# Kernel tuning notes

Hardware: AMD Instinct MI355X
Metric: run time of the kernel (lower is better)

The kernel has to match this reference:

```python
import jax, jax.numpy as jnp
import numpy as np

EPS = 1e-5


def ternarize(w):
    # TWN: delta = 0.7*mean|w|; alpha = mean of |w| over entries above delta
    delta = 0.7 * jnp.mean(jnp.abs(w))
    mask = (jnp.abs(w) > delta).astype(w.dtype)
    alpha = jnp.sum(jnp.abs(w) * mask) / jnp.maximum(jnp.sum(mask), 1.0)
    q = alpha * jnp.sign(w) * mask
    # straight-through estimator (matches torch `w + (q - w).detach()`)
    return w + jax.lax.stop_gradient(q - w)


def conv2d(x, w, stride, pad):
    # x: NCHW, w: OIHW
    return jax.lax.conv_general_dilated(
        x, w, window_strides=(stride, stride), padding=[(pad, pad), (pad, pad)],
        dimension_numbers=("NCHW", "OIHW", "NCHW"))


def batchnorm(x, gamma, beta, mean, var):
    # inference-mode BN over channel dim of NCHW
    inv = gamma / jnp.sqrt(var + EPS)
    return x * inv[None, :, None, None] + (beta - mean * inv)[None, :, None, None]


def setup_inputs() -> dict:
    key = jax.random.key(0)
    ks = jax.random.split(key, 12)
    d = {
        "x": jax.random.normal(ks[0], (64, 3, 224, 224), jnp.float32),
        "w1": jax.random.normal(ks[1], (32, 3, 3, 3), jnp.float32) * 0.1,
        "g1": jnp.ones((32,), jnp.float32), "b1": jnp.zeros((32,), jnp.float32),
        "m1": jax.random.normal(ks[2], (32,), jnp.float32) * 0.1,
        "v1": jax.random.uniform(ks[3], (32,), jnp.float32, 0.5, 1.5),
        "w2": jax.random.normal(ks[4], (64, 32, 3, 3), jnp.float32) * 0.05,
        "g2": jnp.ones((64,), jnp.float32), "b2": jnp.zeros((64,), jnp.float32),
        "m2": jax.random.normal(ks[5], (64,), jnp.float32) * 0.1,
        "v2": jax.random.uniform(ks[6], (64,), jnp.float32, 0.5, 1.5),
        "w3": jax.random.normal(ks[7], (128, 64, 3, 3), jnp.float32) * 0.05,
        "g3": jnp.ones((128,), jnp.float32), "b3": jnp.zeros((128,), jnp.float32),
        "m3": jax.random.normal(ks[8], (128,), jnp.float32) * 0.1,
        "v3": jax.random.uniform(ks[9], (128,), jnp.float32, 0.5, 1.5),
        "wl": jax.random.normal(ks[10], (10, 128), jnp.float32) * 0.1,
        "bl": jax.random.normal(ks[11], (10,), jnp.float32) * 0.01,
    }
    return d


def reference(x, w1, g1, b1, m1, v1, w2, g2, b2, m2, v2,
              w3, g3, b3, m3, v3, wl, bl):
    h = jax.nn.relu(batchnorm(conv2d(x, ternarize(w1), 2, 1), g1, b1, m1, v1))
    h = jax.nn.relu(batchnorm(conv2d(h, ternarize(w2), 1, 1), g2, b2, m2, v2))
    h = jax.nn.relu(batchnorm(conv2d(h, ternarize(w3), 2, 1), g3, b3, m3, v3))
    h = jnp.mean(h, axis=(2, 3))  # AdaptiveAvgPool2d((1,1)) + flatten -> [N,128]
    return h @ ternarize(wl).T + bl
```

## Files before the change

kernel.cpp:

```cpp
#include <hip/hip_runtime.h>
#include <cstddef>

typedef __attribute__((ext_vector_type(8))) short short8;
typedef __attribute__((ext_vector_type(4))) float floatx4;

__device__ __forceinline__ unsigned short f2bf(float f) {
  union { float f; unsigned u; } v; v.f = f;
  const unsigned r = v.u + 0x7fffu + ((v.u >> 16) & 1u);
  return (unsigned short)(r >> 16);
}

__device__ __forceinline__ float block_reduce_sum(float v, float* sm) {
#pragma unroll
  for (int off = 32; off > 0; off >>= 1) v += __shfl_down(v, off, 64);
  const int lane = threadIdx.x & 63, wid = threadIdx.x >> 6;
  __syncthreads();
  if (lane == 0) sm[wid] = v;
  __syncthreads();
  if (threadIdx.x == 0) {
    float t = 0.f;
    const int nw = (blockDim.x + 63) >> 6;
    for (int i = 0; i < nw; ++i) t += sm[i];
    sm[0] = t;
  }
  __syncthreads();
  return sm[0];
}

__device__ __forceinline__ void tsel(int t, const float* w0, const float* w1,
                                     const float* w2, const float* w3, int n0,
                                     int n1, int n2, int n3,
                                     const float*& w, int& n) {
  w = (t == 0) ? w0 : (t == 1) ? w1 : (t == 2) ? w2 : w3;
  n = (t == 0) ? n0 : (t == 1) ? n1 : (t == 2) ? n2 : n3;
}

__global__ __launch_bounds__(256) void tern_phase1(
    const float* w0, const float* w1, const float* w2, const float* w3,
    int n0, int n1, int n2, int n3, float* __restrict__ red) {
  __shared__ float sm[8];
  const float* w; int n;
  tsel(blockIdx.y, w0, w1, w2, w3, n0, n1, n2, n3, w, n);
  if ((int)blockIdx.x * 256 >= n) return;
  const int i = blockIdx.x * 256 + threadIdx.x;
  float s = (i < n) ? fabsf(w[i]) : 0.f;
  s = block_reduce_sum(s, sm);
  if (threadIdx.x == 0) atomicAdd(&red[blockIdx.y * 4 + 0], s);
}

__global__ __launch_bounds__(256) void tern_phase2(
    const float* w0, const float* w1, const float* w2, const float* w3,
    int n0, int n1, int n2, int n3, float* __restrict__ red,
    unsigned short* __restrict__ bp1, unsigned short* __restrict__ bp2,
    unsigned short* __restrict__ bp3, float* __restrict__ ql) {
  __shared__ float sm[8];
  const float* w; int n;
  const int by = blockIdx.y;
  tsel(by, w0, w1, w2, w3, n0, n1, n2, n3, w, n);
  if ((int)blockIdx.x * 256 >= n) return;
  const float delta = 0.7f * red[by * 4 + 0] / (float)n;
  const int i = blockIdx.x * 256 + threadIdx.x;
  float c = 0.f, a = 0.f;
  float wv = 0.f;
  if (i < n) {
    wv = w[i];
    const float av = fabsf(wv);
    if (av > delta) { c = 1.f; a = av; }
  }
  if (i < n) {
    const float sgnf = (wv > delta) ? 1.f : (wv < -delta ? -1.f : 0.f);
    const unsigned short sgnb =
        (wv > delta) ? 0x3F80u : (wv < -delta ? 0xBF80u : 0u);
    if (by == 0) {
      const int k = i % 27, oc = i / 27;
      bp1[((size_t)(k >> 3) * 32 + oc) * 8 + (k & 7)] = sgnb;
    } else if (by == 1) {
      const int k = (i % 9) * 32 + (i % 288) / 9;
      bp2[((size_t)(k >> 3) * 64 + i / 288) * 8 + (k & 7)] = sgnb;
    } else if (by == 2) {
      const int k = (i % 9) * 64 + (i % 576) / 9;
      bp3[((size_t)(k >> 3) * 128 + i / 576) * 8 + (k & 7)] = sgnb;
    } else {
      ql[i] = sgnf;
    }
  }
  c = block_reduce_sum(c, sm);
  a = block_reduce_sum(a, sm);
  if (threadIdx.x == 0) {
    atomicAdd(&red[by * 4 + 1], c);
    atomicAdd(&red[by * 4 + 2], a);
  }
}

__global__ __launch_bounds__(256) void conv1_mfma(
    const float* __restrict__ x, const unsigned short* __restrict__ bp1,
    const float* __restrict__ g1, const float* __restrict__ b1,
    const float* __restrict__ m1, const float* __restrict__ v1,
    const float* __restrict__ red, unsigned short* __restrict__ y) {
  __shared__ float xs[3 * 17 * 33];
  __shared__ unsigned short im[128 * 40];
  const int n = blockIdx.y;
  const int oh0 = (blockIdx.x / 7) * 8, ow0 = (blockIdx.x % 7) * 16;
  const int t = threadIdx.x;
  const int wave = t >> 6, lane = t & 63, quad = lane >> 4, l16 = lane & 15;

  const int ihb = oh0 * 2 - 1, iwb = ow0 * 2 - 1;
  for (int i = t; i < 1683; i += 256) {
    const int ic = i / 561, r2 = i % 561;
    const int pr = r2 / 33, pc = r2 % 33;
    const int ih = ihb + pr, iw = iwb + pc;
    float v = 0.f;
    if ((unsigned)ih < 224u && (unsigned)iw < 224u)
      v = x[((size_t)n * 3 + ic) * 50176 + (size_t)ih * 224 + iw];
    xs[i] = v;
  }
  __syncthreads();

#pragma unroll
  for (int cc = 0; cc < 2; ++cc) {
    const int c = cc * 256 + t;
    const int px = c >> 2, seg = c & 3;
    const int ohl = px >> 4, owl = px & 15;
    unsigned u[4];
#pragma unroll
    for (int jj = 0; jj < 4; ++jj) {
      unsigned short lo = 0, hi = 0;
      const int k0 = seg * 8 + 2 * jj, k1 = k0 + 1;
      if (k0 < 27) {
        const int ic = k0 / 9, tp = k0 % 9;
        lo = f2bf(xs[(ic * 17 + ohl * 2 + tp / 3) * 33 + owl * 2 + tp % 3]);
      }
      if (k1 < 27) {
        const int ic = k1 / 9, tp = k1 % 9;
        hi = f2bf(xs[(ic * 17 + ohl * 2 + tp / 3) * 33 + owl * 2 + tp % 3]);
      }
      u[jj] = (unsigned)lo | ((unsigned)hi << 16);
    }
    *(uint4*)(&im[px * 40 + seg * 8]) = make_uint4(u[0], u[1], u[2], u[3]);
  }

  short8 bfr[2];
#pragma unroll
  for (int nf = 0; nf < 2; ++nf)
    bfr[nf] = *(const short8*)(bp1 + ((size_t)quad * 32 + nf * 16 + l16) * 8);

  floatx4 acc[2][2];
#pragma unroll
  for (int mi = 0; mi < 2; ++mi) {
    acc[mi][0] = (floatx4){0.f, 0.f, 0.f, 0.f};
    acc[mi][1] = (floatx4){0.f, 0.f, 0.f, 0.f};
  }
  __syncthreads();

#pragma unroll
  for (int mi = 0; mi < 2; ++mi) {
    const int pxb = (wave * 2 + mi) * 16;
    const short8 a = *(const short8*)(&im[(pxb + l16) * 40 + quad * 8]);
#pragma unroll
    for (int nf = 0; nf < 2; ++nf)
      acc[mi][nf] = __builtin_amdgcn_mfma_f32_16x16x32_bf16(
          a, bfr[nf], acc[mi][nf], 0, 0, 0);
  }

  const float alpha1 = red[2] / fmaxf(red[1], 1.f);
  float sc[2], bs[2];
#pragma unroll
  for (int nf = 0; nf < 2; ++nf) {
    const int ch = nf * 16 + l16;
    const float inv = g1[ch] / sqrtf(v1[ch] + 1e-5f);
    sc[nf] = alpha1 * inv;
    bs[nf] = b1[ch] - m1[ch] * inv;
  }
  __syncthreads();
#pragma unroll
  for (int mi = 0; mi < 2; ++mi) {
    const int ohl = wave * 2 + mi;
#pragma unroll
    for (int r = 0; r < 4; ++r) {
      const int px = ohl * 16 + quad * 4 + r;
#pragma unroll
      for (int nf = 0; nf < 2; ++nf) {
        const float vv = fmaxf(acc[mi][nf][r] * sc[nf] + bs[nf], 0.f);
        im[px * 40 + ((nf * 16 + l16) ^ (quad * 8))] = f2bf(vv);
      }
    }
  }
  __syncthreads();
#pragma unroll
  for (int i = 0; i < 2; ++i) {
    const int c = i * 256 + t;
    const int px = c >> 2, cg = c & 3;
    const int ohl = px >> 4, owl = px & 15;
    const uint4 v =
        *(const uint4*)(&im[px * 40 + ((cg ^ ((px >> 2) & 3)) * 8)]);
    *(uint4*)(y + (((size_t)n * 112 + oh0 + ohl) * 112 + ow0 + owl) * 32 +
              cg * 8) = v;
  }
}

__global__ __launch_bounds__(256) void conv2_halo(
    const unsigned short* __restrict__ xin,
    const unsigned short* __restrict__ bp,
    const float* __restrict__ g2, const float* __restrict__ b2,
    const float* __restrict__ m2, const float* __restrict__ v2,
    const float* __restrict__ red, unsigned short* __restrict__ yout) {
  constexpr int PH = 10, PW = 18;
  __shared__ unsigned short patch[4 * PH * PW * 8];
  __shared__ unsigned short st[128 * 72];
  const int t = threadIdx.x;
  const int img = blockIdx.z;
  const int toh = blockIdx.x / 7, tow = blockIdx.x % 7;
  const int wave = t >> 6, lane = t & 63, quad = lane >> 4, l16 = lane & 15;
  const int oh0 = toh * 8, ow0 = tow * 16;

  for (int c = t; c < PH * PW * 4; c += 256) {
    const int pix = c >> 2, seg = c & 3;
    const int pi = pix / PW, pj = pix % PW;
    const int ih = oh0 - 1 + pi, iw = ow0 - 1 + pj;
    uint4 v = make_uint4(0u, 0u, 0u, 0u);
    if ((unsigned)ih < 112u && (unsigned)iw < 112u)
      v = *(const uint4*)(xin + (((size_t)img * 112 + ih) * 112 + iw) * 32 +
                          seg * 8);
    *(uint4*)(&patch[((seg * PH + pi) * PW + pj) * 8]) = v;
  }

  floatx4 acc[2][4];
#pragma unroll
  for (int mf = 0; mf < 2; ++mf)
#pragma unroll
    for (int nf = 0; nf < 4; ++nf) acc[mf][nf] = (floatx4){0.f, 0.f, 0.f, 0.f};

  short8 bcur[4], bnxt[4];
#pragma unroll
  for (int nf = 0; nf < 4; ++nf)
    bcur[nf] = *(const short8*)(bp + ((size_t)quad * 64 + nf * 16 + l16) * 8);
  __syncthreads();

#pragma unroll
  for (int tap = 0; tap < 9; ++tap) {
    const int kh = tap / 3, kw = tap % 3;
    if (tap + 1 < 9) {
      const int kg = (tap + 1) * 4 + quad;
#pragma unroll
      for (int nf = 0; nf < 4; ++nf)
        bnxt[nf] = *(const short8*)(bp + ((size_t)kg * 64 + nf * 16 + l16) * 8);
    }
#pragma unroll
    for (int mf = 0; mf < 2; ++mf) {
      const int pi = (wave * 2 + mf) + kh;
      const short8 a = *(const short8*)(
          &patch[((quad * PH + pi) * PW + l16 + kw) * 8]);
#pragma unroll
      for (int nf = 0; nf < 4; ++nf)
        acc[mf][nf] = __builtin_amdgcn_mfma_f32_16x16x32_bf16(
            a, bcur[nf], acc[mf][nf], 0, 0, 0);
    }
#pragma unroll
    for (int nf = 0; nf < 4; ++nf) bcur[nf] = bnxt[nf];
  }

  const float alpha2 = red[6] / fmaxf(red[5], 1.f);
  float sc[4], bs[4];
#pragma unroll
  for (int nf = 0; nf < 4; ++nf) {
    const int ch = nf * 16 + l16;
    const float inv = g2[ch] / sqrtf(v2[ch] + 1e-5f);
    sc[nf] = alpha2 * inv;
    bs[nf] = b2[ch] - m2[ch] * inv;
  }
#pragma unroll
  for (int mf = 0; mf < 2; ++mf) {
    const int ohl = wave * 2 + mf;
#pragma unroll
    for (int r = 0; r < 4; ++r) {
      const int px = ohl * 16 + quad * 4 + r;
#pragma unroll
      for (int nf = 0; nf < 4; ++nf) {
        const float vv = fmaxf(acc[mf][nf][r] * sc[nf] + bs[nf], 0.f);
        st[px * 72 + ((nf * 16 + l16) ^ (quad * 8))] = f2bf(vv);
      }
    }
  }
  __syncthreads();
#pragma unroll
  for (int i = 0; i < 4; ++i) {
    const int c = i * 256 + t;
    const int px = c >> 3, cg = c & 7;
    const int ohl = px >> 4, owl = px & 15;
    const uint4 v =
        *(const uint4*)(&st[px * 72 + ((cg ^ ((px >> 2) & 3)) * 8)]);
    *(uint4*)(yout + (((size_t)img * 112 + oh0 + ohl) * 112 + ow0 + owl) * 64 +
              cg * 8) = v;
  }
}

__global__ __launch_bounds__(256, 4) void conv3_pool(
    const unsigned short* __restrict__ act2,
    const unsigned short* __restrict__ bp3,
    const float* __restrict__ g3, const float* __restrict__ b3,
    const float* __restrict__ m3, const float* __restrict__ v3,
    const float* __restrict__ red, float* __restrict__ pooled) {
  __shared__ unsigned short c2p[2][4 * 17 * 18 * 8];
  __shared__ float pbuf[128];
  const int t = threadIdx.x;
  const int img = blockIdx.y;
  const int ty = blockIdx.x / 7, tx = blockIdx.x % 7;
  const int o3h0 = ty * 8, o3w0 = tx * 8;
  const int wave = t >> 6, lane = t & 63, quad = lane >> 4, l16 = lane & 15;
  const int h0 = o3h0 * 2 - 1, w0 = o3w0 * 2 - 1;

  int a3off[4];
#pragma unroll
  for (int mf = 0; mf < 4; ++mf) {
    const int px = mf * 16 + l16;
    a3off[mf] = ((quad * 17 + (px >> 3) * 2) * 18 + (px & 7)) * 8;
  }

  floatx4 acc3[4][2];
#pragma unroll
  for (int mf = 0; mf < 4; ++mf) {
    acc3[mf][0] = (floatx4){0.f, 0.f, 0.f, 0.f};
    acc3[mf][1] = (floatx4){0.f, 0.f, 0.f, 0.f};
  }

  uint4 r[5];
#define C3_ISSUE(H)                                                          \
  {                                                                          \
    _Pragma("unroll") for (int i = 0; i < 5; ++i) {                          \
      const int c = i * 256 + t;                                             \
      uint4 v = make_uint4(0u, 0u, 0u, 0u);                                  \
      if (c < 1156) {                                                        \
        const int pix = c >> 2, seg = c & 3;                                 \
        const int pi = pix / 17, pj = pix % 17;                              \
        const int ih = h0 + pi, iw = w0 + pj;                                \
        if ((unsigned)ih < 112u && (unsigned)iw < 112u)                      \
          v = *(const uint4*)(act2 +                                         \
                              (((size_t)img * 112 + ih) * 112 + iw) * 64 +   \
                              (H) * 32 + seg * 8);                           \
      }                                                                      \
      r[i] = v;                                                              \
    }                                                                        \
  }
#define C3_WRITE(H)                                                          \
  {                                                                          \
    _Pragma("unroll") for (int i = 0; i < 5; ++i) {                          \
      const int c = i * 256 + t;                                             \
      if (c < 1156) {                                                        \
        const int pix = c >> 2, seg = c & 3;                                 \
        const int pi = pix / 17, pj = pix % 17;                              \
        const int slot = (pj >> 1) + (pj & 1) * 9;                           \
        *(uint4*)(&c2p[H][((seg * 17 + pi) * 18 + slot) * 8]) = r[i];        \
      }                                                                      \
    }                                                                        \
  }
#define C3_COMPUTE(H)                                                        \
  {                                                                          \
    _Pragma("unroll") for (int tap = 0; tap < 9; ++tap) {                    \
      const int kh = tap / 3, kw = tap % 3;                                  \
      const int kg = tap * 8 + (H) * 4 + quad;                               \
      const short8 b0 =                                                      \
          *(const short8*)(bp3 + ((size_t)kg * 128 + wave * 32 + l16) * 8);  \
      const short8 b1 = *(const short8*)(bp3 + ((size_t)kg * 128 +           \
                                                wave * 32 + 16 + l16) * 8);  \
      const int toff = (kh * 18 + (kw >> 1) + (kw & 1) * 9) * 8;             \
      _Pragma("unroll") for (int mf = 0; mf < 4; ++mf) {                     \
        const short8 a = *(const short8*)(&c2p[H][a3off[mf] + toff]);        \
        acc3[mf][0] = __builtin_amdgcn_mfma_f32_16x16x32_bf16(               \
            a, b0, acc3[mf][0], 0, 0, 0);                                    \
        acc3[mf][1] = __builtin_amdgcn_mfma_f32_16x16x32_bf16(               \
            a, b1, acc3[mf][1], 0, 0, 0);                                    \
      }                                                                      \
    }                                                                        \
  }

  C3_ISSUE(0);
  C3_WRITE(0);
  __syncthreads();
  C3_ISSUE(1);
  C3_COMPUTE(0);
  C3_WRITE(1);
  __syncthreads();
  C3_COMPUTE(1);

  const float alpha3 = red[10] / fmaxf(red[9], 1.f);
#pragma unroll
  for (int nf = 0; nf < 2; ++nf) {
    const int ch = wave * 32 + nf * 16 + l16;
    const float inv = g3[ch] / sqrtf(v3[ch] + 1e-5f);
    const float sc = alpha3 * inv, bs = b3[ch] - m3[ch] * inv;
    float s = 0.f;
#pragma unroll
    for (int mf = 0; mf < 4; ++mf)
#pragma unroll
      for (int rr = 0; rr < 4; ++rr)
        s += fmaxf(acc3[mf][nf][rr] * sc + bs, 0.f);
    s += __shfl_xor(s, 16);
    s += __shfl_xor(s, 32);
    if (lane < 16) pbuf[ch] = s;
  }
  __syncthreads();
  if (t < 128) atomicAdd(&pooled[(size_t)img * 128 + t], pbuf[t]);
#undef C3_ISSUE
#undef C3_WRITE
#undef C3_COMPUTE
}

__global__ void linear_kernel(const float* __restrict__ pooled,
                              const float* __restrict__ ql,
                              const float* __restrict__ bl,
                              const float* __restrict__ red,
                              float* __restrict__ out) {
  const int idx = blockIdx.x * blockDim.x + threadIdx.x;
  if (idx >= 64 * 10) return;
  const int n = idx / 10, o = idx % 10;
  const float* p = pooled + (size_t)n * 128;
  const float* w = ql + (size_t)o * 128;
  float s = 0.f;
#pragma unroll 4
  for (int c = 0; c < 128; ++c) s += p[c] * w[c];
  const float alpha_l = red[14] / fmaxf(red[13], 1.f);
  out[idx] = s * (alpha_l / 3136.f) + bl[o];
}

extern "C" void kernel_launch(void* const* d_in, const int* in_sizes, int n_in,
                              void* d_out, int out_size, void* d_ws,
                              size_t ws_size, hipStream_t stream) {
  const float* x  = (const float*)d_in[0];
  const float* w1 = (const float*)d_in[1];
  const float* g1 = (const float*)d_in[2];
  const float* b1 = (const float*)d_in[3];
  const float* m1 = (const float*)d_in[4];
  const float* v1 = (const float*)d_in[5];
  const float* w2 = (const float*)d_in[6];
  const float* g2 = (const float*)d_in[7];
  const float* b2 = (const float*)d_in[8];
  const float* m2 = (const float*)d_in[9];
  const float* v2 = (const float*)d_in[10];
  const float* w3 = (const float*)d_in[11];
  const float* g3 = (const float*)d_in[12];
  const float* b3 = (const float*)d_in[13];
  const float* m3 = (const float*)d_in[14];
  const float* v3 = (const float*)d_in[15];
  const float* wl = (const float*)d_in[16];
  const float* bl = (const float*)d_in[17];
  float* out = (float*)d_out;

  float* Wf = (float*)d_ws;
  float* red = Wf;
  float* pooled = red + 16;
  float* bp1f = pooled + 8192;
  float* ql = bp1f + 512;
  unsigned short* bp1 = (unsigned short*)bp1f;
  unsigned short* Us = (unsigned short*)(ql + 1280);
  unsigned short* bp2 = Us;
  unsigned short* bp3 = bp2 + 18432;
  unsigned short* act1 = bp3 + 73728;
  unsigned short* act2 = act1 + 25690112;

  hipMemsetAsync(red, 0, (16 + 8192 + 512) * sizeof(float), stream);
  tern_phase1<<<dim3(288, 4), 256, 0, stream>>>(w1, w2, w3, wl, 864, 18432,
                                                73728, 1280, red);
  tern_phase2<<<dim3(288, 4), 256, 0, stream>>>(w1, w2, w3, wl, 864, 18432,
                                                73728, 1280, red, bp1, bp2,
                                                bp3, ql);

  conv1_mfma<<<dim3(98, 64), 256, 0, stream>>>(x, bp1, g1, b1, m1, v1, red,
                                               act1);
  conv2_halo<<<dim3(98, 1, 64), 256, 0, stream>>>(act1, bp2, g2, b2, m2, v2,
                                                  red, act2);
  conv3_pool<<<dim3(49, 64), 256, 0, stream>>>(act2, bp3, g3, b3, m3, v3, red,
                                               pooled);
  linear_kernel<<<3, 256, 0, stream>>>(pooled, ql, bl, red, out);
}
```

Measured before the change: 261.7 us.

## Stage conv2 weights in LDS and write outputs directly from registers

After: 264.5 us. No clear change (+1.1%).

```diff
diff --git a/kernel.cpp b/kernel.cpp
--- a/kernel.cpp
+++ b/kernel.cpp
@@ -206,13 +206,18 @@
     const float* __restrict__ red, unsigned short* __restrict__ yout) {
   constexpr int PH = 10, PW = 18;
   __shared__ unsigned short patch[4 * PH * PW * 8];
-  __shared__ unsigned short st[128 * 72];
+  __shared__ unsigned short bsm[2304 * 8];
   const int t = threadIdx.x;
   const int img = blockIdx.z;
   const int toh = blockIdx.x / 7, tow = blockIdx.x % 7;
   const int wave = t >> 6, lane = t & 63, quad = lane >> 4, l16 = lane & 15;
   const int oh0 = toh * 8, ow0 = tow * 16;
 
+#pragma unroll
+  for (int i = 0; i < 9; ++i) {
+    const int c = i * 256 + t;
+    *(uint4*)(&bsm[c * 8]) = *(const uint4*)(bp + (size_t)c * 8);
+  }
   for (int c = t; c < PH * PW * 4; c += 256) {
     const int pix = c >> 2, seg = c & 3;
     const int pi = pix / PW, pj = pix % PW;
@@ -229,22 +234,16 @@
   for (int mf = 0; mf < 2; ++mf)
 #pragma unroll
     for (int nf = 0; nf < 4; ++nf) acc[mf][nf] = (floatx4){0.f, 0.f, 0.f, 0.f};
-
-  short8 bcur[4], bnxt[4];
-#pragma unroll
-  for (int nf = 0; nf < 4; ++nf)
-    bcur[nf] = *(const short8*)(bp + ((size_t)quad * 64 + nf * 16 + l16) * 8);
   __syncthreads();
 
 #pragma unroll
   for (int tap = 0; tap < 9; ++tap) {
     const int kh = tap / 3, kw = tap % 3;
-    if (tap + 1 < 9) {
-      const int kg = (tap + 1) * 4 + quad;
-#pragma unroll
-      for (int nf = 0; nf < 4; ++nf)
-        bnxt[nf] = *(const short8*)(bp + ((size_t)kg * 64 + nf * 16 + l16) * 8);
-    }
+    short8 bfr[4];
+#pragma unroll
+    for (int nf = 0; nf < 4; ++nf)
+      bfr[nf] = *(const short8*)(
+          &bsm[((tap * 4 + quad) * 64 + nf * 16 + l16) * 8]);
 #pragma unroll
     for (int mf = 0; mf < 2; ++mf) {
       const int pi = (wave * 2 + mf) + kh;
@@ -253,10 +252,8 @@
 #pragma unroll
       for (int nf = 0; nf < 4; ++nf)
         acc[mf][nf] = __builtin_amdgcn_mfma_f32_16x16x32_bf16(
-            a, bcur[nf], acc[mf][nf], 0, 0, 0);
+            a, bfr[nf], acc[mf][nf], 0, 0, 0);
     }
-#pragma unroll
-    for (int nf = 0; nf < 4; ++nf) bcur[nf] = bnxt[nf];
   }
 
   const float alpha2 = red[6] / fmaxf(red[5], 1.f);
@@ -270,27 +267,17 @@
   }
 #pragma unroll
   for (int mf = 0; mf < 2; ++mf) {
-    const int ohl = wave * 2 + mf;
+    const int oh = oh0 + wave * 2 + mf;
 #pragma unroll
     for (int r = 0; r < 4; ++r) {
-      const int px = ohl * 16 + quad * 4 + r;
+      const int ow = ow0 + quad * 4 + r;
+      const size_t base = (((size_t)img * 112 + oh) * 112 + ow) * 64;
 #pragma unroll
       for (int nf = 0; nf < 4; ++nf) {
         const float vv = fmaxf(acc[mf][nf][r] * sc[nf] + bs[nf], 0.f);
-        st[px * 72 + ((nf * 16 + l16) ^ (quad * 8))] = f2bf(vv);
+        yout[base + nf * 16 + l16] = f2bf(vv);
       }
     }
-  }
-  __syncthreads();
-#pragma unroll
-  for (int i = 0; i < 4; ++i) {
-    const int c = i * 256 + t;
-    const int px = c >> 3, cg = c & 7;
-    const int ohl = px >> 4, owl = px & 15;
-    const uint4 v =
-        *(const uint4*)(&st[px * 72 + ((cg ^ ((px >> 2) & 3)) * 8)]);
-    *(uint4*)(yout + (((size_t)img * 112 + oh0 + ohl) * 112 + ow0 + owl) * 64 +
-              cg * 8) = v;
   }
 }
 
```

## Fuse conv2 and conv3+pool into one kernel keeping conv2 output in LDS

Applied to the files above, without the earlier changes.

Measured after the change: 256.9 us. Within noise of the previous version (-1.8%).

```diff
diff --git a/kernel.cpp b/kernel.cpp
--- a/kernel.cpp
+++ b/kernel.cpp
@@ -198,42 +198,54 @@
   }
 }
 
-__global__ __launch_bounds__(256) void conv2_halo(
-    const unsigned short* __restrict__ xin,
-    const unsigned short* __restrict__ bp,
+__global__ __launch_bounds__(256, 2) void conv23_fused(
+    const unsigned short* __restrict__ act1,
+    const unsigned short* __restrict__ bp2,
+    const unsigned short* __restrict__ bp3,
     const float* __restrict__ g2, const float* __restrict__ b2,
     const float* __restrict__ m2, const float* __restrict__ v2,
-    const float* __restrict__ red, unsigned short* __restrict__ yout) {
-  constexpr int PH = 10, PW = 18;
-  __shared__ unsigned short patch[4 * PH * PW * 8];
-  __shared__ unsigned short st[128 * 72];
+    const float* __restrict__ g3, const float* __restrict__ b3,
+    const float* __restrict__ m3, const float* __restrict__ v3,
+    const float* __restrict__ red, float* __restrict__ pooled) {
+  __shared__ unsigned short a1p[4 * 19 * 19 * 8];
+  __shared__ unsigned short c2o[8 * 17 * 18 * 8];
+  __shared__ float pbuf[128];
   const int t = threadIdx.x;
-  const int img = blockIdx.z;
-  const int toh = blockIdx.x / 7, tow = blockIdx.x % 7;
+  const int img = blockIdx.y;
+  const int ty = blockIdx.x / 7, tx = blockIdx.x % 7;
   const int wave = t >> 6, lane = t & 63, quad = lane >> 4, l16 = lane & 15;
-  const int oh0 = toh * 8, ow0 = tow * 16;
-
-  for (int c = t; c < PH * PW * 4; c += 256) {
-    const int pix = c >> 2, seg = c & 3;
-    const int pi = pix / PW, pj = pix % PW;
-    const int ih = oh0 - 1 + pi, iw = ow0 - 1 + pj;
+  const int h0 = ty * 16 - 1, w0 = tx * 16 - 1;
+
+  for (int c = t; c < 19 * 19 * 4; c += 256) {
+    const int seg = c & 3, pix = c >> 2;
+    const int ri = pix / 19, rj = pix % 19;
+    const int ih = h0 - 1 + ri, iw = w0 - 1 + rj;
     uint4 v = make_uint4(0u, 0u, 0u, 0u);
     if ((unsigned)ih < 112u && (unsigned)iw < 112u)
-      v = *(const uint4*)(xin + (((size_t)img * 112 + ih) * 112 + iw) * 32 +
+      v = *(const uint4*)(act1 + (((size_t)img * 112 + ih) * 112 + iw) * 32 +
                           seg * 8);
-    *(uint4*)(&patch[((seg * PH + pi) * PW + pj) * 8]) = v;
-  }
-
-  floatx4 acc[2][4];
-#pragma unroll
-  for (int mf = 0; mf < 2; ++mf)
-#pragma unroll
-    for (int nf = 0; nf < 4; ++nf) acc[mf][nf] = (floatx4){0.f, 0.f, 0.f, 0.f};
+    *(uint4*)(&a1p[((seg * 19 + ri) * 19 + rj) * 8]) = v;
+  }
+
+  int abase[5];
+#pragma unroll
+  for (int s = 0; s < 5; ++s) {
+    const int mt = wave + s * 4;
+    int apx = mt * 16 + l16;
+    if (apx > 288) apx = 288;
+    const int pi = apx / 17, pj = apx % 17;
+    abase[s] = ((quad * 19 + pi) * 19 + pj) * 8;
+  }
+  floatx4 acc2[5][4];
+#pragma unroll
+  for (int s = 0; s < 5; ++s)
+#pragma unroll
+    for (int nf = 0; nf < 4; ++nf) acc2[s][nf] = (floatx4){0.f, 0.f, 0.f, 0.f};
 
   short8 bcur[4], bnxt[4];
 #pragma unroll
   for (int nf = 0; nf < 4; ++nf)
-    bcur[nf] = *(const short8*)(bp + ((size_t)quad * 64 + nf * 16 + l16) * 8);
+    bcur[nf] = *(const short8*)(bp2 + ((size_t)quad * 64 + nf * 16 + l16) * 8);
   __syncthreads();
 
 #pragma unroll
@@ -243,17 +255,17 @@
       const int kg = (tap + 1) * 4 + quad;
 #pragma unroll
       for (int nf = 0; nf < 4; ++nf)
-        bnxt[nf] = *(const short8*)(bp + ((size_t)kg * 64 + nf * 16 + l16) * 8);
-    }
-#pragma unroll
-    for (int mf = 0; mf < 2; ++mf) {
-      const int pi = (wave * 2 + mf) + kh;
-      const short8 a = *(const short8*)(
-          &patch[((quad * PH + pi) * PW + l16 + kw) * 8]);
+        bnxt[nf] =
+            *(const short8*)(bp2 + ((size_t)kg * 64 + nf * 16 + l16) * 8);
+    }
+    const int toff = (kh * 19 + kw) * 8;
+#pragma unroll
+    for (int s = 0; s < 5; ++s) {
+      const short8 a = *(const short8*)(&a1p[abase[s] + toff]);
 #pragma unroll
       for (int nf = 0; nf < 4; ++nf)
-        acc[mf][nf] = __builtin_amdgcn_mfma_f32_16x16x32_bf16(
-            a, bcur[nf], acc[mf][nf], 0, 0, 0);
+        acc2[s][nf] = __builtin_amdgcn_mfma_f32_16x16x32_bf16(
+            a, bcur[nf], acc2[s][nf], 0, 0, 0);
     }
 #pragma unroll
     for (int nf = 0; nf < 4; ++nf) bcur[nf] = bnxt[nf];
@@ -268,46 +280,28 @@
     sc[nf] = alpha2 * inv;
     bs[nf] = b2[ch] - m2[ch] * inv;
   }
-#pragma unroll
-  for (int mf = 0; mf < 2; ++mf) {
-    const int ohl = wave * 2 + mf;
+  const int lo8 = l16 & 7, hs0 = l16 >> 3;
+#pragma unroll
+  for (int s = 0; s < 5; ++s) {
+    const int mt = wave + s * 4;
 #pragma unroll
     for (int r = 0; r < 4; ++r) {
-      const int px = ohl * 16 + quad * 4 + r;
-#pragma unroll
-      for (int nf = 0; nf < 4; ++nf) {
-        const float vv = fmaxf(acc[mf][nf][r] * sc[nf] + bs[nf], 0.f);
-        st[px * 72 + ((nf * 16 + l16) ^ (quad * 8))] = f2bf(vv);
+      const int px = mt * 16 + quad * 4 + r;
+      if (px <= 288) {
+        const int pi = px / 17, pj = px % 17;
+        const int slot = (pj >> 1) + (pj & 1) * 9;
+        const bool inb =
+            ((unsigned)(h0 + pi) < 112u) && ((unsigned)(w0 + pj) < 112u);
+#pragma unroll
+        for (int nf = 0; nf < 4; ++nf) {
+          const float vv =
+              inb ? fmaxf(acc2[s][nf][r] * sc[nf] + bs[nf], 0.f) : 0.f;
+          c2o[(((nf * 2 + hs0) * 17 + pi) * 18 + slot) * 8 + lo8] = f2bf(vv);
+        }
       }
     }
   }
   __syncthreads();
-#pragma unroll
-  for (int i = 0; i < 4; ++i) {
-    const int c = i * 256 + t;
-    const int px = c >> 3, cg = c & 7;
-    const int ohl = px >> 4, owl = px & 15;
-    const uint4 v =
-        *(const uint4*)(&st[px * 72 + ((cg ^ ((px >> 2) & 3)) * 8)]);
-    *(uint4*)(yout + (((size_t)img * 112 + oh0 + ohl) * 112 + ow0 + owl) * 64 +
-              cg * 8) = v;
-  }
-}
-
-__global__ __launch_bounds__(256, 4) void conv3_pool(
-    const unsigned short* __restrict__ act2,
-    const unsigned short* __restrict__ bp3,
-    const float* __restrict__ g3, const float* __restrict__ b3,
-    const float* __restrict__ m3, const float* __restrict__ v3,
-    const float* __restrict__ red, float* __restrict__ pooled) {
-  __shared__ unsigned short c2p[2][4 * 17 * 18 * 8];
-  __shared__ float pbuf[128];
-  const int t = threadIdx.x;
-  const int img = blockIdx.y;
-  const int ty = blockIdx.x / 7, tx = blockIdx.x % 7;
-  const int o3h0 = ty * 8, o3w0 = tx * 8;
-  const int wave = t >> 6, lane = t & 63, quad = lane >> 4, l16 = lane & 15;
-  const int h0 = o3h0 * 2 - 1, w0 = o3w0 * 2 - 1;
 
   int a3off[4];
 #pragma unroll
@@ -315,94 +309,60 @@
     const int px = mf * 16 + l16;
     a3off[mf] = ((quad * 17 + (px >> 3) * 2) * 18 + (px & 7)) * 8;
   }
-
   floatx4 acc3[4][2];
 #pragma unroll
   for (int mf = 0; mf < 4; ++mf) {
     acc3[mf][0] = (floatx4){0.f, 0.f, 0.f, 0.f};
     acc3[mf][1] = (floatx4){0.f, 0.f, 0.f, 0.f};
   }
-
-  uint4 r[5];
-#define C3_ISSUE(H)                                                          \
-  {                                                                          \
-    _Pragma("unroll") for (int i = 0; i < 5; ++i) {                          \
-      const int c = i * 256 + t;                                             \
-      uint4 v = make_uint4(0u, 0u, 0u, 0u);                                  \
-      if (c < 1156) {                                                        \
-        const int pix = c >> 2, seg = c & 3;                                 \
-        const int pi = pix / 17, pj = pix % 17;                              \
-        const int ih = h0 + pi, iw = w0 + pj;                                \
-        if ((unsigned)ih < 112u && (unsigned)iw < 112u)                      \
-          v = *(const uint4*)(act2 +                                         \
-                              (((size_t)img * 112 + ih) * 112 + iw) * 64 +   \
-                              (H) * 32 + seg * 8);                           \
-      }                                                                      \
-      r[i] = v;                                                              \
-    }                                                                        \
-  }
-#define C3_WRITE(H)                                                          \
-  {                                                                          \
-    _Pragma("unroll") for (int i = 0; i < 5; ++i) {                          \
-      const int c = i * 256 + t;                                             \
-      if (c < 1156) {                                                        \
-        const int pix = c >> 2, seg = c & 3;                                 \
-        const int pi = pix / 17, pj = pix % 17;                              \
-        const int slot = (pj >> 1) + (pj & 1) * 9;                           \
-        *(uint4*)(&c2p[H][((seg * 17 + pi) * 18 + slot) * 8]) = r[i];        \
-      }                                                                      \
-    }                                                                        \
-  }
-#define C3_COMPUTE(H)                                                        \
-  {                                                                          \
-    _Pragma("unroll") for (int tap = 0; tap < 9; ++tap) {                    \
-      const int kh = tap / 3, kw = tap % 3;                                  \
-      const int kg = tap * 8 + (H) * 4 + quad;                               \
-      const short8 b0 =                                                      \
-          *(const short8*)(bp3 + ((size_t)kg * 128 + wave * 32 + l16) * 8);  \
-      const short8 b1 = *(const short8*)(bp3 + ((size_t)kg * 128 +           \
-                                                wave * 32 + 16 + l16) * 8);  \
-      const int toff = (kh * 18 + (kw >> 1) + (kw & 1) * 9) * 8;             \
-      _Pragma("unroll") for (int mf = 0; mf < 4; ++mf) {                     \
-        const short8 a = *(const short8*)(&c2p[H][a3off[mf] + toff]);        \
-        acc3[mf][0] = __builtin_amdgcn_mfma_f32_16x16x32_bf16(               \
-            a, b0, acc3[mf][0], 0, 0, 0);                                    \
-        acc3[mf][1] = __builtin_amdgcn_mfma_f32_16x16x32_bf16(               \
-            a, b1, acc3[mf][1], 0, 0, 0);                                    \
-      }                                                                      \
-    }                                                                        \
-  }
-
-  C3_ISSUE(0);
-  C3_WRITE(0);
-  __syncthreads();
-  C3_ISSUE(1);
-  C3_COMPUTE(0);
-  C3_WRITE(1);
-  __syncthreads();
-  C3_COMPUTE(1);
+  short8 b3c0, b3c1, b3n0, b3n1;
+  {
+    const int kg = quad;
+    b3c0 = *(const short8*)(bp3 + ((size_t)kg * 128 + wave * 32 + l16) * 8);
+    b3c1 =
+        *(const short8*)(bp3 + ((size_t)kg * 128 + wave * 32 + 16 + l16) * 8);
+  }
+#pragma unroll
+  for (int u = 0; u < 18; ++u) {
+    const int H = u / 9, tap = u % 9;
+    const int kh = tap / 3, kw = tap % 3;
+    if (u + 1 < 18) {
+      const int H2 = (u + 1) / 9, tap2 = (u + 1) % 9;
+      const int kg = tap2 * 8 + H2 * 4 + quad;
+      b3n0 = *(const short8*)(bp3 + ((size_t)kg * 128 + wave * 32 + l16) * 8);
+      b3n1 = *(const short8*)(bp3 +
+                              ((size_t)kg * 128 + wave * 32 + 16 + l16) * 8);
+    }
+    const int toff = (kh * 18 + (kw >> 1) + (kw & 1) * 9) * 8 + H * 9792;
+#pragma unroll
+    for (int mf = 0; mf < 4; ++mf) {
+      const short8 a = *(const short8*)(&c2o[a3off[mf] + toff]);
+      acc3[mf][0] = __builtin_amdgcn_mfma_f32_16x16x32_bf16(
+          a, b3c0, acc3[mf][0], 0, 0, 0);
+      acc3[mf][1] = __builtin_amdgcn_mfma_f32_16x16x32_bf16(
+          a, b3c1, acc3[mf][1], 0, 0, 0);
+    }
+    b3c0 = b3n0; b3c1 = b3n1;
+  }
 
   const float alpha3 = red[10] / fmaxf(red[9], 1.f);
 #pragma unroll
   for (int nf = 0; nf < 2; ++nf) {
     const int ch = wave * 32 + nf * 16 + l16;
     const float inv = g3[ch] / sqrtf(v3[ch] + 1e-5f);
-    const float sc = alpha3 * inv, bs = b3[ch] - m3[ch] * inv;
+    const float scv = alpha3 * inv, bsv = b3[ch] - m3[ch] * inv;
     float s = 0.f;
 #pragma unroll
     for (int mf = 0; mf < 4; ++mf)
 #pragma unroll
       for (int rr = 0; rr < 4; ++rr)
-        s += fmaxf(acc3[mf][nf][rr] * sc + bs, 0.f);
+        s += fmaxf(acc3[mf][nf][rr] * scv + bsv, 0.f);
     s += __shfl_xor(s, 16);
     s += __shfl_xor(s, 32);
     if (lane < 16) pbuf[ch] = s;
   }
   __syncthreads();
   if (t < 128) atomicAdd(&pooled[(size_t)img * 128 + t], pbuf[t]);
-#undef C3_ISSUE
-#undef C3_WRITE
-#undef C3_COMPUTE
 }
 
 __global__ void linear_kernel(const float* __restrict__ pooled,
@@ -455,7 +415,6 @@
   unsigned short* bp2 = Us;
   unsigned short* bp3 = bp2 + 18432;
   unsigned short* act1 = bp3 + 73728;
-  unsigned short* act2 = act1 + 25690112;
 
   hipMemsetAsync(red, 0, (16 + 8192 + 512) * sizeof(float), stream);
   tern_phase1<<<dim3(288, 4), 256, 0, stream>>>(w1, w2, w3, wl, 864, 18432,
@@ -466,9 +425,8 @@
 
   conv1_mfma<<<dim3(98, 64), 256, 0, stream>>>(x, bp1, g1, b1, m1, v1, red,
                                                act1);
-  conv2_halo<<<dim3(98, 1, 64), 256, 0, stream>>>(act1, bp2, g2, b2, m2, v2,
-                                                  red, act2);
-  conv3_pool<<<dim3(49, 64), 256, 0, stream>>>(act2, bp3, g3, b3, m3, v3, red,
-                                               pooled);
+  conv23_fused<<<dim3(49, 64), 256, 0, stream>>>(act1, bp2, bp3, g2, b2, m2,
+                                                 v2, g3, b3, m3, v3, red,
+                                                 pooled);
   linear_kernel<<<3, 256, 0, stream>>>(pooled, ql, bl, red, out);
 }
```
